# Kernel optimization log

Measured on AMD Instinct MI355X. Metric: run time of the kernel, lower is better.

The kernel has to match this reference:

```python
import jax, jax.numpy as jnp
import numpy as np

B, C, W, H = 4, 256, 64, 64
D = C // 8  # reduced query/key channels


def setup_inputs() -> dict:
    key = jax.random.key(0)
    k1, k2, k3, k4, k5 = jax.random.split(key, 5)
    return {
        "x": jax.random.normal(k1, (B, C, W, H), dtype=jnp.float32),
        "q_weight": jax.random.normal(k2, (D, C), dtype=jnp.float32) * 0.05,
        "k_weight": jax.random.normal(k3, (D, C), dtype=jnp.float32) * 0.05,
        "v_weight": jax.random.normal(k4, (C, C), dtype=jnp.float32) * 0.05,
        "gamma": jax.random.normal(k5, (1,), dtype=jnp.float32),
    }


def reference(x, q_weight, k_weight, v_weight, gamma):
    b, c, w, h = x.shape
    n = w * h
    xf = x.reshape(b, c, n)                       # (B, C, N)
    # 1x1 convs == channel matmuls
    q = jnp.einsum('dc,bcn->bdn', q_weight, xf)   # (B, D, N)
    k = jnp.einsum('dc,bcn->bdn', k_weight, xf)   # (B, D, N)
    v = jnp.einsum('oc,bcn->bon', v_weight, xf)   # (B, C, N)
    # energy[b, i, j] = <q[:, i], k[:, j]>  (unscaled, single head)
    energy = jnp.einsum('bdi,bdj->bij', q, k)     # (B, N, N)
    attn = jax.nn.softmax(energy, axis=-1)        # softmax over keys j
    # out[b, c, i] = sum_j v[b, c, j] * attn[b, i, j]
    out = jnp.einsum('bcj,bij->bci', v, attn)     # (B, C, N)
    out = out.reshape(b, c, w, h)
    return gamma[0] * out + x
```

## Files before the change

kernel.cpp:

```cpp
#include <hip/hip_runtime.h>
#include <math.h>

#define Bb 4
#define Cc 256
#define Nn 4096
#define Dd 32
#define CH 128
#define NJ 32
#define PST 136
#define XST 264

typedef __attribute__((ext_vector_type(8))) short bf16x8;
typedef __attribute__((ext_vector_type(4))) float f32x4;

union bfp { bf16x8 v; uint4 q; };

__device__ __forceinline__ unsigned pk2r(float a, float b) {
    unsigned au = __builtin_bit_cast(unsigned, a) + 0x8000u;
    unsigned bu = __builtin_bit_cast(unsigned, b) + 0x8000u;
    return __builtin_amdgcn_perm(bu, au, 0x07060302u);
}
__device__ __forceinline__ void load_lds16(const void* g, void* l) {
    __builtin_amdgcn_global_load_lds(
        (const __attribute__((address_space(1))) void*)g,
        (__attribute__((address_space(3))) void*)l, 16, 0, 0);
}
__device__ __forceinline__ float fexp2(float x) {
#if __has_builtin(__builtin_amdgcn_exp2f)
    return __builtin_amdgcn_exp2f(x);
#else
    return __exp2f(x);
#endif
}
template <int CTRL>
__device__ __forceinline__ float dppf(float v) {
    int iv = __builtin_bit_cast(int, v);
    return __builtin_bit_cast(float,
        __builtin_amdgcn_update_dpp(iv, iv, CTRL, 0xF, 0xF, false));
}
__device__ __forceinline__ float rowsum16(float v) {
    v += dppf<0xB1>(v);
    v += dppf<0x4E>(v);
    v += dppf<0x141>(v);
    v += dppf<0x140>(v);
    return v;
}

__global__ __launch_bounds__(256) void pack_w(
    const float* __restrict__ qw, const float* __restrict__ kw,
    const float* __restrict__ vw, short* __restrict__ wpk) {
    const int g = blockIdx.x * 256 + threadIdx.x;
    const int qd = g & 3, m = (g >> 2) & 15, kc = (g >> 6) & 7, ot = g >> 9;
    const int o = 16 * ot + m;
    const float* src; float sc = 1.0f;
    if (o < 32)      { src = qw + (size_t)o * Cc; sc = 1.44269504088896f; }
    else if (o < 64) { src = kw + (size_t)(o - 32) * Cc; }
    else             { src = vw + (size_t)(o - 64) * Cc; }
    const float* s8 = src + 32 * kc + 8 * qd;
    uint4 u;
    u.x = pk2r(s8[0] * sc, s8[1] * sc);
    u.y = pk2r(s8[2] * sc, s8[3] * sc);
    u.z = pk2r(s8[4] * sc, s8[5] * sc);
    u.w = pk2r(s8[6] * sc, s8[7] * sc);
    *(uint4*)(wpk + (size_t)g * 8) = u;
}

__global__ __launch_bounds__(256) void proj(
    const float* __restrict__ x, const short* __restrict__ wpk,
    short* __restrict__ q_t, short* __restrict__ k_t, short* __restrict__ v_b) {
    __shared__ alignas(16) short xs[32 * XST];
    const int b = blockIdx.z;
    const int n0 = blockIdx.x * 32;
    const int tid = threadIdx.x;
    const int w = tid >> 6;
    const int lane = tid & 63, qd = lane >> 4, m = lane & 15;

    {
        const int n = tid & 31, cgx = tid >> 5;
        const float* xp = x + ((size_t)b * Cc + 32 * cgx) * Nn + n0 + n;
        float xv[32];
#pragma unroll
        for (int i = 0; i < 32; ++i) xv[i] = xp[(size_t)i * Nn];
        short* row = xs + n * XST + 32 * cgx;
#pragma unroll
        for (int u4 = 0; u4 < 4; ++u4)
            *(uint4*)(row + 8 * u4) = make_uint4(
                pk2r(xv[8*u4+0], xv[8*u4+1]), pk2r(xv[8*u4+2], xv[8*u4+3]),
                pk2r(xv[8*u4+4], xv[8*u4+5]), pk2r(xv[8*u4+6], xv[8*u4+7]));
    }
    __syncthreads();

    const int fslot = m * 4 + qd;
    f32x4 acc[5][2];
#pragma unroll
    for (int i = 0; i < 5; ++i)
#pragma unroll
        for (int nt = 0; nt < 2; ++nt) acc[i][nt] = (f32x4){0.f, 0.f, 0.f, 0.f};

    bfp afc[5], afn[5];
#pragma unroll
    for (int i = 0; i < 5; ++i)
        afc[i].q = *(const uint4*)(wpk + ((size_t)((4*i + w) * 8) * 64 + fslot) * 8);

    for (int kc = 0; kc < 8; ++kc) {
        if (kc < 7) {
#pragma unroll
            for (int i = 0; i < 5; ++i)
                afn[i].q = *(const uint4*)(
                    wpk + ((size_t)((4*i + w) * 8 + kc + 1) * 64 + fslot) * 8);
        }
        bfp b0, b1;
        b0.q = *(const uint4*)&xs[(     m) * XST + 32 * kc + 8 * qd];
        b1.q = *(const uint4*)&xs[(16 + m) * XST + 32 * kc + 8 * qd];
#pragma unroll
        for (int i = 0; i < 5; ++i)
            acc[i][0] = __builtin_amdgcn_mfma_f32_16x16x32_bf16(afc[i].v, b0.v, acc[i][0], 0, 0, 0);
#pragma unroll
        for (int i = 0; i < 5; ++i)
            acc[i][1] = __builtin_amdgcn_mfma_f32_16x16x32_bf16(afc[i].v, b1.v, acc[i][1], 0, 0, 0);
#pragma unroll
        for (int i = 0; i < 5; ++i) afc[i] = afn[i];
    }

#pragma unroll
    for (int i = 0; i < 5; ++i) {
        const int ot = 4 * i + w;
        if (ot < 4) {
            short* dst = (ot < 2 ? q_t : k_t) + (size_t)b * Nn * Dd;
            const int dbase = (ot & 1) * 16 + 4 * qd;
#pragma unroll
            for (int nt = 0; nt < 2; ++nt) {
                const f32x4 a = acc[i][nt];
                *(uint2*)(dst + (size_t)(n0 + 16 * nt + m) * Dd + dbase) =
                    make_uint2(pk2r(a[0], a[1]), pk2r(a[2], a[3]));
            }
        } else {
            const int crow = (ot - 4) * 16 + 4 * qd;
            const int gbase = n0 & ~63;
            const int off2 = (n0 & 32) ? 2 : 0;
#pragma unroll
            for (int rr = 0; rr < 4; ++rr) {
                const unsigned pv = pk2r(acc[i][0][rr], acc[i][1][rr]);
                *(unsigned*)(v_b + ((size_t)b * Cc + crow + rr) * Nn +
                             gbase + 4 * m + off2) = pv;
            }
        }
    }
}

__global__ __launch_bounds__(256, 2) void attn(
    const float* __restrict__ x, const short* __restrict__ q_t,
    const short* __restrict__ k_t, const short* __restrict__ v_b,
    const float* __restrict__ gamma, float* __restrict__ out) {
    __shared__ alignas(16) char pool[34304];
    short* k0s   = (short*)(pool);
    short* k1s   = (short*)(pool + 8192);
    short* p_s   = (short*)(pool + 16384);
    float* l_red = (float*)(pool + 33792);
    float* o_red = (float*)(pool);

    const int bid = blockIdx.x;
    const int b = (bid & 7) >> 1, cg = bid & 1;
    const int i0 = (bid >> 3) * 64;
    const int tid = threadIdx.x;
    const int w = tid >> 6, lane = tid & 63;
    const int qd = lane >> 4, m = lane & 15;
    const int g  = w >> 1;
    const int ch = w & 1;
    const int mtS = 2 * ch;

    const short* ktb = k_t + (size_t)b * Nn * Dd;
    const short* vtb = v_b + ((size_t)(b * Cc) + cg * CH) * Nn;

    bfp af[2];
#pragma unroll
    for (int mtl = 0; mtl < 2; ++mtl)
        af[mtl].q = *(const uint4*)(
            q_t + ((size_t)b * Nn + i0 + 16 * (mtS + mtl) + m) * Dd + 8 * qd);

    const short* vr[4];
#pragma unroll
    for (int ct = 0; ct < 4; ++ct)
        vr[ct] = vtb + (size_t)(64 * ch + 16 * ct + m) * Nn + 64 * g + 8 * qd;

    load_lds16(ktb + tid * 8, k0s + tid * 8);
    load_lds16(ktb + 2048 + tid * 8, k0s + 2048 + tid * 8);
    uint4 va[8], vc[8];
#pragma unroll
    for (int ct = 0; ct < 4; ++ct) {
        va[2 * ct]     = *(const uint4*)(vr[ct]);
        va[2 * ct + 1] = *(const uint4*)(vr[ct] + 32);
    }

    f32x4 acc[4][4];
#pragma unroll
    for (int mt = 0; mt < 4; ++mt)
#pragma unroll
        for (int ct = 0; ct < 4; ++ct) acc[mt][ct] = (f32x4){0.f, 0.f, 0.f, 0.f};
    float lp[8] = {0.f, 0.f, 0.f, 0.f, 0.f, 0.f, 0.f, 0.f};

    auto body = [&](int jt, const short* kcur, short* knext,
                    uint4* vcur, uint4* vnext) {
        __syncthreads();

        f32x4 sf[2][4];
#pragma unroll
        for (int ntl = 0; ntl < 4; ++ntl) {
            bfp kf;
            kf.q = *(const uint4*)(kcur + (64 * g + 16 * ntl + m) * Dd + 8 * qd);
#pragma unroll
            for (int mtl = 0; mtl < 2; ++mtl)
                sf[mtl][ntl] = __builtin_amdgcn_mfma_f32_16x16x32_bf16(
                    af[mtl].v, kf.v, (f32x4){0.f, 0.f, 0.f, 0.f}, 0, 0, 0);
        }
#pragma unroll
        for (int mtl = 0; mtl < 2; ++mtl)
#pragma unroll
            for (int rr = 0; rr < 4; ++rr) {
                const float p0 = fexp2(sf[mtl][0][rr]);
                const float p1 = fexp2(sf[mtl][1][rr]);
                const float p2 = fexp2(sf[mtl][2][rr]);
                const float p3 = fexp2(sf[mtl][3][rr]);
                lp[4 * mtl + rr] += (p0 + p1) + (p2 + p3);
                const int row = 16 * (mtS + mtl) + 4 * qd + rr;
                *(uint2*)&p_s[row * PST + 64 * g + 4 * m] =
                    make_uint2(pk2r(p0, p1), pk2r(p2, p3));
            }
        __syncthreads();

        if (jt + 1 < NJ) {
            const size_t ko = (size_t)(jt + 1) * 4096;
            load_lds16(ktb + ko + tid * 8, knext + tid * 8);
            load_lds16(ktb + ko + 2048 + tid * 8, knext + 2048 + tid * 8);
            const int joff = 128 * (jt + 1);
#pragma unroll
            for (int ct = 0; ct < 4; ++ct) {
                vnext[2 * ct]     = *(const uint4*)(vr[ct] + joff);
                vnext[2 * ct + 1] = *(const uint4*)(vr[ct] + joff + 32);
            }
        }
#pragma unroll
        for (int kcl = 0; kcl < 2; ++kcl) {
            const int kc = 2 * g + kcl;
            bf16x8 pa[4];
#pragma unroll
            for (int mt = 0; mt < 4; ++mt) {
                bfp t;
                t.q = *(const uint4*)&p_s[(16 * mt + m) * PST + 32 * kc + 8 * qd];
                pa[mt] = t.v;
            }
#pragma unroll
            for (int ct = 0; ct < 4; ++ct) {
                bfp vv; vv.q = vcur[2 * ct + kcl];
#pragma unroll
                for (int mt = 0; mt < 4; ++mt)
                    acc[mt][ct] = __builtin_amdgcn_mfma_f32_16x16x32_bf16(
                        pa[mt], vv.v, acc[mt][ct], 0, 0, 0);
            }
        }
    };

    for (int jt = 0; jt < NJ; jt += 2) {
        body(jt, k0s, k1s, va, vc);
        body(jt + 1, k1s, k0s, vc, va);
    }

#pragma unroll
    for (int mtl = 0; mtl < 2; ++mtl)
#pragma unroll
        for (int rr = 0; rr < 4; ++rr) {
            const float s = rowsum16(lp[4 * mtl + rr]);
            if (m == 0)
                l_red[64 * g + 16 * (mtS + mtl) + 4 * qd + rr] = s;
        }

    __syncthreads();
    if (w < 2) {
#pragma unroll
        for (int mt = 0; mt < 4; ++mt)
#pragma unroll
            for (int ct = 0; ct < 4; ++ct)
#pragma unroll
                for (int rr = 0; rr < 4; ++rr)
                    o_red[(16 * mt + 4 * qd + rr) * 129 + 64 * ch + 16 * ct + m] =
                        acc[mt][ct][rr];
    }
    __syncthreads();
    if (w >= 2) {
#pragma unroll
        for (int mt = 0; mt < 4; ++mt)
#pragma unroll
            for (int ct = 0; ct < 4; ++ct)
#pragma unroll
                for (int rr = 0; rr < 4; ++rr)
                    o_red[(16 * mt + 4 * qd + rr) * 129 + 64 * ch + 16 * ct + m] +=
                        acc[mt][ct][rr];
    }
    __syncthreads();

    const float gm = gamma[0];
    const int i = lane;
    const float linv = 1.0f / (l_red[i] + l_red[64 + i]);
#pragma unroll
    for (int cc = 0; cc < 32; ++cc) {
        const int cl = 32 * w + cc;
        const float val = o_red[i * 129 + cl] * linv;
        const size_t gidx = ((size_t)b * Cc + cg * CH + cl) * Nn + i0 + i;
        out[gidx] = gm * val + x[gidx];
    }
}

extern "C" void kernel_launch(void* const* d_in, const int* in_sizes, int n_in,
                              void* d_out, int out_size, void* d_ws, size_t ws_size,
                              hipStream_t stream) {
    const float* x     = (const float*)d_in[0];
    const float* qw    = (const float*)d_in[1];
    const float* kw    = (const float*)d_in[2];
    const float* vw    = (const float*)d_in[3];
    const float* gamma = (const float*)d_in[4];
    float* out = (float*)d_out;

    short* q_t = (short*)d_ws;
    short* k_t = q_t + (size_t)Bb * Nn * Dd;
    short* v_b = k_t + (size_t)Bb * Nn * Dd;
    short* wpk = v_b + (size_t)Bb * Cc * Nn;

    pack_w<<<dim3(40), 256, 0, stream>>>(qw, kw, vw, wpk);
    proj<<<dim3(Nn / 32, 1, Bb), 256, 0, stream>>>(x, wpk, q_t, k_t, v_b);
    attn<<<dim3(512, 1, 1), 256, 0, stream>>>(x, q_t, k_t, v_b, gamma, out);
}
```

Before: 160.2 us.

## Halve query tile per block and split key columns across warps

The attention kernel now processes 32 query rows per block instead of 64, doubling the grid to 1024 blocks. Each warp owns 32 output channels for all rows, with no cross-warp accumulator reduction. Shared memory drops and launch bounds rise to 4 blocks per CU to increase occupancy and parallelism. In exchange, each K tile and V stream is re-read twice as often per query, doubling K/V global traffic.

```diff
diff --git a/kernel.cpp b/kernel.cpp
--- a/kernel.cpp
+++ b/kernel.cpp
@@ -148,84 +148,77 @@
     }
 }
 
-__global__ __launch_bounds__(256, 2) void attn(
+__global__ __launch_bounds__(256, 4) void attn(
     const float* __restrict__ x, const short* __restrict__ q_t,
     const short* __restrict__ k_t, const short* __restrict__ v_b,
     const float* __restrict__ gamma, float* __restrict__ out) {
-    __shared__ alignas(16) char pool[34304];
+    __shared__ alignas(16) char pool[25344];
     short* k0s   = (short*)(pool);
     short* k1s   = (short*)(pool + 8192);
     short* p_s   = (short*)(pool + 16384);
-    float* l_red = (float*)(pool + 33792);
-    float* o_red = (float*)(pool);
+    float* l_red = (float*)(pool + 25088);
+    float* o_t   = (float*)(pool);
 
     const int bid = blockIdx.x;
-    const int b = (bid & 7) >> 1, cg = bid & 1;
-    const int i0 = (bid >> 3) * 64;
+    const int bcg = bid >> 7, it = bid & 127;
+    const int b = bcg >> 1, cg = bcg & 1;
+    const int i0 = it * 32;
     const int tid = threadIdx.x;
     const int w = tid >> 6, lane = tid & 63;
     const int qd = lane >> 4, m = lane & 15;
-    const int g  = w >> 1;
-    const int ch = w & 1;
-    const int mtS = 2 * ch;
+    const int mt = w & 1;
+    const int jg = w >> 1;
 
     const short* ktb = k_t + (size_t)b * Nn * Dd;
     const short* vtb = v_b + ((size_t)(b * Cc) + cg * CH) * Nn;
 
-    bfp af[2];
-#pragma unroll
-    for (int mtl = 0; mtl < 2; ++mtl)
-        af[mtl].q = *(const uint4*)(
-            q_t + ((size_t)b * Nn + i0 + 16 * (mtS + mtl) + m) * Dd + 8 * qd);
-
-    const short* vr[4];
-#pragma unroll
-    for (int ct = 0; ct < 4; ++ct)
-        vr[ct] = vtb + (size_t)(64 * ch + 16 * ct + m) * Nn + 64 * g + 8 * qd;
+    bfp af;
+    af.q = *(const uint4*)(q_t + ((size_t)b * Nn + i0 + 16 * mt + m) * Dd + 8 * qd);
+
+    const short* vr[2];
+#pragma unroll
+    for (int ct = 0; ct < 2; ++ct)
+        vr[ct] = vtb + (size_t)(32 * w + 16 * ct + m) * Nn + 8 * qd;
 
     load_lds16(ktb + tid * 8, k0s + tid * 8);
     load_lds16(ktb + 2048 + tid * 8, k0s + 2048 + tid * 8);
     uint4 va[8], vc[8];
 #pragma unroll
-    for (int ct = 0; ct < 4; ++ct) {
-        va[2 * ct]     = *(const uint4*)(vr[ct]);
-        va[2 * ct + 1] = *(const uint4*)(vr[ct] + 32);
-    }
-
-    f32x4 acc[4][4];
-#pragma unroll
-    for (int mt = 0; mt < 4; ++mt)
-#pragma unroll
-        for (int ct = 0; ct < 4; ++ct) acc[mt][ct] = (f32x4){0.f, 0.f, 0.f, 0.f};
-    float lp[8] = {0.f, 0.f, 0.f, 0.f, 0.f, 0.f, 0.f, 0.f};
+    for (int ct = 0; ct < 2; ++ct)
+#pragma unroll
+        for (int kc = 0; kc < 4; ++kc)
+            va[4 * ct + kc] = *(const uint4*)(vr[ct] + 32 * kc);
+
+    f32x4 acc[2][2];
+#pragma unroll
+    for (int mtl = 0; mtl < 2; ++mtl)
+#pragma unroll
+        for (int ct = 0; ct < 2; ++ct) acc[mtl][ct] = (f32x4){0.f, 0.f, 0.f, 0.f};
+    float lp[4] = {0.f, 0.f, 0.f, 0.f};
 
     auto body = [&](int jt, const short* kcur, short* knext,
                     uint4* vcur, uint4* vnext) {
         __syncthreads();
 
-        f32x4 sf[2][4];
+        f32x4 sf[4];
 #pragma unroll
         for (int ntl = 0; ntl < 4; ++ntl) {
             bfp kf;
-            kf.q = *(const uint4*)(kcur + (64 * g + 16 * ntl + m) * Dd + 8 * qd);
-#pragma unroll
-            for (int mtl = 0; mtl < 2; ++mtl)
-                sf[mtl][ntl] = __builtin_amdgcn_mfma_f32_16x16x32_bf16(
-                    af[mtl].v, kf.v, (f32x4){0.f, 0.f, 0.f, 0.f}, 0, 0, 0);
-        }
-#pragma unroll
-        for (int mtl = 0; mtl < 2; ++mtl)
-#pragma unroll
-            for (int rr = 0; rr < 4; ++rr) {
-                const float p0 = fexp2(sf[mtl][0][rr]);
-                const float p1 = fexp2(sf[mtl][1][rr]);
-                const float p2 = fexp2(sf[mtl][2][rr]);
-                const float p3 = fexp2(sf[mtl][3][rr]);
-                lp[4 * mtl + rr] += (p0 + p1) + (p2 + p3);
-                const int row = 16 * (mtS + mtl) + 4 * qd + rr;
-                *(uint2*)&p_s[row * PST + 64 * g + 4 * m] =
-                    make_uint2(pk2r(p0, p1), pk2r(p2, p3));
-            }
+            kf.q = *(const uint4*)(kcur + (64 * jg + 16 * ntl + m) * Dd + 8 * qd);
+            sf[ntl] = __builtin_amdgcn_mfma_f32_16x16x32_bf16(
+                af.v, kf.v, (f32x4){0.f, 0.f, 0.f, 0.f}, 0, 0, 0);
+        }
+#pragma unroll
+        for (int rr = 0; rr < 4; ++rr) {
+            const float p0 = fexp2(sf[0][rr]);
+            const float p1 = fexp2(sf[1][rr]);
+            const float p2 = fexp2(sf[2][rr]);
+            const float p3 = fexp2(sf[3][rr]);
+            lp[rr] += (p0 + p1) + (p2 + p3);
+            const int row = 16 * mt + 4 * qd + rr;
+            *(uint2*)&p_s[row * PST + 64 * jg + 4 * m] =
+                make_uint2(pk2r(p0, p1), pk2r(p2, p3));
+        }
         __syncthreads();
 
         if (jt + 1 < NJ) {
@@ -234,28 +227,27 @@
             load_lds16(ktb + ko + 2048 + tid * 8, knext + 2048 + tid * 8);
             const int joff = 128 * (jt + 1);
 #pragma unroll
-            for (int ct = 0; ct < 4; ++ct) {
-                vnext[2 * ct]     = *(const uint4*)(vr[ct] + joff);
-                vnext[2 * ct + 1] = *(const uint4*)(vr[ct] + joff + 32);
+            for (int ct = 0; ct < 2; ++ct)
+#pragma unroll
+                for (int kc = 0; kc < 4; ++kc)
+                    vnext[4 * ct + kc] = *(const uint4*)(vr[ct] + joff + 32 * kc);
+        }
+#pragma unroll
+        for (int kc = 0; kc < 4; ++kc) {
+            bf16x8 pa[2];
+#pragma unroll
+            for (int mtl = 0; mtl < 2; ++mtl) {
+                bfp t;
+                t.q = *(const uint4*)&p_s[(16 * mtl + m) * PST + 32 * kc + 8 * qd];
+                pa[mtl] = t.v;
             }
-        }
-#pragma unroll
-        for (int kcl = 0; kcl < 2; ++kcl) {
-            const int kc = 2 * g + kcl;
-            bf16x8 pa[4];
-#pragma unroll
-            for (int mt = 0; mt < 4; ++mt) {
-                bfp t;
-                t.q = *(const uint4*)&p_s[(16 * mt + m) * PST + 32 * kc + 8 * qd];
-                pa[mt] = t.v;
-            }
-#pragma unroll
-            for (int ct = 0; ct < 4; ++ct) {
-                bfp vv; vv.q = vcur[2 * ct + kcl];
-#pragma unroll
-                for (int mt = 0; mt < 4; ++mt)
-                    acc[mt][ct] = __builtin_amdgcn_mfma_f32_16x16x32_bf16(
-                        pa[mt], vv.v, acc[mt][ct], 0, 0, 0);
+#pragma unroll
+            for (int ct = 0; ct < 2; ++ct) {
+                bfp vv; vv.q = vcur[4 * ct + kc];
+#pragma unroll
+                for (int mtl = 0; mtl < 2; ++mtl)
+                    acc[mtl][ct] = __builtin_amdgcn_mfma_f32_16x16x32_bf16(
+                        pa[mtl], vv.v, acc[mtl][ct], 0, 0, 0);
             }
         }
     };
@@ -266,45 +258,29 @@
     }
 
 #pragma unroll
+    for (int rr = 0; rr < 4; ++rr) {
+        const float s = rowsum16(lp[rr]);
+        if (m == 0) l_red[32 * jg + 16 * mt + 4 * qd + rr] = s;
+    }
+
+    __syncthreads();
+#pragma unroll
     for (int mtl = 0; mtl < 2; ++mtl)
 #pragma unroll
-        for (int rr = 0; rr < 4; ++rr) {
-            const float s = rowsum16(lp[4 * mtl + rr]);
-            if (m == 0)
-                l_red[64 * g + 16 * (mtS + mtl) + 4 * qd + rr] = s;
-        }
-
+        for (int ct = 0; ct < 2; ++ct)
+#pragma unroll
+            for (int rr = 0; rr < 4; ++rr)
+                o_t[(16 * mtl + 4 * qd + rr) * 132 + 32 * w + 16 * ct + m] =
+                    acc[mtl][ct][rr];
     __syncthreads();
-    if (w < 2) {
-#pragma unroll
-        for (int mt = 0; mt < 4; ++mt)
-#pragma unroll
-            for (int ct = 0; ct < 4; ++ct)
-#pragma unroll
-                for (int rr = 0; rr < 4; ++rr)
-                    o_red[(16 * mt + 4 * qd + rr) * 129 + 64 * ch + 16 * ct + m] =
-                        acc[mt][ct][rr];
-    }
-    __syncthreads();
-    if (w >= 2) {
-#pragma unroll
-        for (int mt = 0; mt < 4; ++mt)
-#pragma unroll
-            for (int ct = 0; ct < 4; ++ct)
-#pragma unroll
-                for (int rr = 0; rr < 4; ++rr)
-                    o_red[(16 * mt + 4 * qd + rr) * 129 + 64 * ch + 16 * ct + m] +=
-                        acc[mt][ct][rr];
-    }
-    __syncthreads();
 
     const float gm = gamma[0];
-    const int i = lane;
-    const float linv = 1.0f / (l_red[i] + l_red[64 + i]);
-#pragma unroll
-    for (int cc = 0; cc < 32; ++cc) {
-        const int cl = 32 * w + cc;
-        const float val = o_red[i * 129 + cl] * linv;
+    const int i = tid & 31, cch = tid >> 5;
+    const float linv = 1.0f / (l_red[i] + l_red[32 + i]);
+#pragma unroll
+    for (int cc = 0; cc < 16; ++cc) {
+        const int cl = cch * 16 + cc;
+        const float val = o_t[i * 132 + cl] * linv;
         const size_t gidx = ((size_t)b * Cc + cg * CH + cl) * Nn + i0 + i;
         out[gidx] = gm * val + x[gidx];
     }
@@ -327,5 +303,5 @@
 
     pack_w<<<dim3(40), 256, 0, stream>>>(qw, kw, vw, wpk);
     proj<<<dim3(Nn / 32, 1, Bb), 256, 0, stream>>>(x, wpk, q_t, k_t, v_b);
-    attn<<<dim3(512, 1, 1), 256, 0, stream>>>(x, q_t, k_t, v_b, gamma, out);
-}
+    attn<<<dim3(1024, 1, 1), 256, 0, stream>>>(x, q_t, k_t, v_b, gamma, out);
+}
```

Result: slower. 242.1 us (+51.1%).
